# Optimization experiments

Hardware: AMD Instinct MI355X
Metric: run time of the kernel (lower is better)

Reference implementation:

```python
import jax, jax.numpy as jnp
import numpy as np

B, S, NX = 2, 2048, 1024
N_STATE, N_HEAD = 1024, 16
HEAD_DIM = N_STATE // N_HEAD


def setup_inputs() -> dict:
    key = jax.random.key(0)
    k1, k2, k3 = jax.random.split(key, 3)
    x = jax.random.normal(k1, (B, S, NX), dtype=jnp.float32)
    w_c = jax.random.normal(k2, (NX, 3 * N_STATE), dtype=jnp.float32) * 0.02
    b_c = jnp.zeros((3 * N_STATE,), dtype=jnp.float32)
    w_p = jax.random.normal(k3, (NX, N_STATE), dtype=jnp.float32) * 0.02
    b_p = jnp.zeros((N_STATE,), dtype=jnp.float32)
    return {"x": x, "w_c": w_c, "b_c": b_c, "w_p": w_p, "b_p": b_p}


def reference(x, w_c, b_c, w_p, b_p):
    # c_attn: 1x1 conv == dense over last dim -> [B, S, 3*n_state]
    c = jnp.einsum('bsn,nf->bsf', x, w_c) + b_c
    q, k, v = jnp.split(c, 3, axis=2)

    def split_heads(t):  # [B,S,n_state] -> [B,H,S,D]
        return t.reshape(B, S, N_HEAD, HEAD_DIM).transpose(0, 2, 1, 3)

    q = split_heads(q)
    k = split_heads(k)  # we contract over D directly instead of transposing to [B,H,D,S]
    v = split_heads(v)

    # scores [B,H,S,S], scaled by rsqrt(head_dim) (scale=True)
    w = jnp.einsum('bhqd,bhkd->bhqk', q, k) * jax.lax.rsqrt(jnp.float32(HEAD_DIM))
    # band mask exactly as in source: w*b + -1e9*(1-b)
    band = jnp.tril(jnp.ones((S, S), dtype=jnp.float32))[None, None]
    w = w * band + (-1e9) * (1.0 - band)
    w = jax.nn.softmax(w, axis=-1)
    a = jnp.einsum('bhqk,bhkd->bhqd', w, v)

    # merge heads -> [B,S,n_state]
    a = a.transpose(0, 2, 1, 3).reshape(B, S, N_STATE)
    # c_proj
    out = jnp.einsum('bsn,nf->bsf', a, w_p) + b_p
    return out
```

## Files before the change

### kernel.cpp

```cpp
#include <hip/hip_runtime.h>
#include <math.h>

#define BATCH 2
#define SEQ 2048
#define NX 1024
#define NSTATE 1024
#define NHEAD 16
#define HDIM 64
#define QKV_LD (3*NSTATE)

typedef __attribute__((ext_vector_type(4))) float f32x4;
typedef __attribute__((ext_vector_type(8))) short bf16x8;

__device__ __forceinline__ unsigned short f2bf(float x) {
    unsigned int u = __float_as_uint(x);
    u = (u + 0x7FFFu + ((u >> 16) & 1u)) >> 16;
    return (unsigned short)u;
}

#define GLL(src, dst) __builtin_amdgcn_global_load_lds( \
    (const __attribute__((address_space(1))) void*)(src), \
    (__attribute__((address_space(3))) void*)(dst), 16, 0, 0)

__global__ __launch_bounds__(256) void prep_kernel(
    const float* __restrict__ x, const float* __restrict__ w_c,
    const float* __restrict__ w_p,
    unsigned short* __restrict__ xbf, unsigned short* __restrict__ wcT,
    unsigned short* __restrict__ wpT)
{
    const int bx = blockIdx.x;
    const int t = threadIdx.x;
    if (bx < 4096) {
        int i = bx * 256 + t;
        float4 v = ((const float4*)x)[i];
        ushort4 o;
        o.x = f2bf(v.x); o.y = f2bf(v.y); o.z = f2bf(v.z); o.w = f2bf(v.w);
        ((ushort4*)xbf)[i] = o;
        return;
    }
    __shared__ float tile[64][65];
    const float* in;
    unsigned short* out;
    int R, C, c0, r0;
    if (bx < 4096 + 768) {
        int idx = bx - 4096;
        in = w_c; out = wcT; R = NX; C = 3 * NSTATE;
        c0 = (idx % 48) * 64; r0 = (idx / 48) * 64;
    } else {
        int idx = bx - 4864;
        in = w_p; out = wpT; R = NX; C = NSTATE;
        c0 = (idx % 16) * 64; r0 = (idx / 16) * 64;
    }
    const int cc = t & 63;
    const int rb = t >> 6;
    #pragma unroll
    for (int i = 0; i < 16; i++) {
        int rr = rb + i * 4;
        tile[rr][cc] = in[(size_t)(r0 + rr) * C + c0 + cc];
    }
    __syncthreads();
    #pragma unroll
    for (int i = 0; i < 16; i++) {
        int rr = rb + i * 4;
        out[(size_t)(c0 + rr) * R + r0 + cc] = f2bf(tile[cc][rr]);
    }
}

__global__ __launch_bounds__(256) void vtrans_kernel(
    const unsigned short* __restrict__ qkv, unsigned short* __restrict__ vt)
{
    __shared__ unsigned short t[64][72];
    const int s0 = blockIdx.x * 64;
    const int bh = blockIdx.y;
    const int b = bh >> 4, h = bh & 15;
    const int r = threadIdx.x >> 2;
    const int cg = (threadIdx.x & 3) * 16;
    const unsigned short* src = qkv + (size_t)(b * SEQ + s0 + r) * QKV_LD
                                + 2 * NSTATE + h * HDIM + cg;
    *(bf16x8*)&t[r][cg]     = *(const bf16x8*)src;
    *(bf16x8*)&t[r][cg + 8] = *(const bf16x8*)(src + 8);
    __syncthreads();
    unsigned short tmp[16];
    #pragma unroll
    for (int i = 0; i < 16; i++) tmp[i] = t[cg + i][r];
    unsigned short* dst = vt + (size_t)(bh * 64 + r) * SEQ + s0 + cg;
    *(bf16x8*)dst       = ((const bf16x8*)tmp)[0];
    *(bf16x8*)(dst + 8) = ((const bf16x8*)tmp)[1];
}

template<bool BF16_OUT>
__global__ __launch_bounds__(256) void gemm_bf16(
    const unsigned short* __restrict__ A,
    const unsigned short* __restrict__ BT,
    const float* __restrict__ bias,
    void* __restrict__ Cv, int M, int N, int K)
{
    __shared__ unsigned short Als[128 * 32];
    __shared__ unsigned short Bls[128 * 32];
    const int tid = threadIdx.x;
    const int wave = tid >> 6, lane = tid & 63;
    const int bm = blockIdx.x * 128, bn = blockIdx.y * 128;
    const int wr = (wave >> 1) * 64, wc = (wave & 1) * 64;

    f32x4 acc[4][4];
    #pragma unroll
    for (int m = 0; m < 4; m++)
        #pragma unroll
        for (int n = 0; n < 4; n++)
            acc[m][n] = (f32x4){0.f, 0.f, 0.f, 0.f};

    const int arow = tid >> 2;
    const int ac8 = (tid & 3) * 8;
    char* alds0 = (char*)Als + wave * 1024;
    char* blds0 = (char*)Bls + wave * 1024;
    const int fr = lane & 15, kq = (lane >> 4) * 8;

    for (int k0 = 0; k0 < K; k0 += 32) {
        const unsigned short* ga0 = A  + (size_t)(bm + arow) * K + k0 + ac8;
        const unsigned short* gb0 = BT + (size_t)(bn + arow) * K + k0 + ac8;
        GLL(ga0, alds0);
        GLL(ga0 + (size_t)64 * K, alds0 + 4096);
        GLL(gb0, blds0);
        GLL(gb0 + (size_t)64 * K, blds0 + 4096);
        __syncthreads();

        bf16x8 af[4], bfr[4];
        #pragma unroll
        for (int m = 0; m < 4; m++)
            af[m] = *(const bf16x8*)&Als[(wr + m * 16 + fr) * 32 + kq];
        #pragma unroll
        for (int n = 0; n < 4; n++)
            bfr[n] = *(const bf16x8*)&Bls[(wc + n * 16 + fr) * 32 + kq];
        #pragma unroll
        for (int m = 0; m < 4; m++)
            #pragma unroll
            for (int n = 0; n < 4; n++)
                acc[m][n] = __builtin_amdgcn_mfma_f32_16x16x32_bf16(
                    af[m], bfr[n], acc[m][n], 0, 0, 0);
        __syncthreads();
    }

    const int cr = (lane >> 4) * 4;
    const int ccol = lane & 15;
    #pragma unroll
    for (int m = 0; m < 4; m++) {
        const int row = bm + wr + m * 16 + cr;
        #pragma unroll
        for (int n = 0; n < 4; n++) {
            const int col = bn + wc + n * 16 + ccol;
            const float bv = bias[col];
            #pragma unroll
            for (int j = 0; j < 4; j++) {
                float v = acc[m][n][j] + bv;
                if (BF16_OUT)
                    ((unsigned short*)Cv)[(size_t)(row + j) * N + col] = f2bf(v);
                else
                    ((float*)Cv)[(size_t)(row + j) * N + col] = v;
            }
        }
    }
}

__global__ __launch_bounds__(256) void attn_mfma(
    const unsigned short* __restrict__ qkv,
    const unsigned short* __restrict__ vt,
    unsigned short* __restrict__ a_out)
{
    const int qb = (int)gridDim.x - 1 - (int)blockIdx.x;
    const int h = blockIdx.y, b = blockIdx.z;
    const int tid = threadIdx.x;
    const int w = tid >> 6, lane = tid & 63;
    const int c = lane & 15, hh = lane >> 4;

    __shared__ unsigned short Kls[2 * 64 * 64];
    __shared__ unsigned short Vls[2 * 64 * 64];
    __shared__ unsigned short Pls[4][16 * 64];

    const size_t qrow = (size_t)(b * SEQ + qb * 64 + w * 16 + c);
    const unsigned short* qp = qkv + qrow * QKV_LD + h * HDIM;
    bf16x8 qf0 = *(const bf16x8*)(qp + hh * 8);
    bf16x8 qf1 = *(const bf16x8*)(qp + 32 + hh * 8);

    f32x4 acc_o[4];
    #pragma unroll
    for (int n = 0; n < 4; n++) acc_o[n] = (f32x4){0.f, 0.f, 0.f, 0.f};
    float m_run = -1e30f, l = 0.f;
    const float Cc = 0.18033688f;

    const int o0 = tid * 16;
    const int r0 = o0 >> 7, sc0 = (o0 & 127) ^ ((r0 & 7) << 4);
    const int o1 = 4096 + tid * 16;
    const int r1 = o1 >> 7, sc1 = (o1 & 127) ^ ((r1 & 7) << 4);

    char* kld = (char*)Kls + w * 1024;
    char* vld = (char*)Vls + w * 1024;
    const char* gkbase = (const char*)(qkv + (size_t)b * SEQ * QKV_LD + NSTATE + h * HDIM);
    const char* gvbase = (const char*)(vt + (size_t)(b * NHEAD + h) * HDIM * SEQ);

    #define STAGE(kt_, buf_) do { \
        const char* gk = gkbase + (size_t)(kt_) * 64 * 6144; \
        const char* gv = gvbase + (size_t)(kt_) * 128; \
        char* kd = kld + (buf_) * 8192; \
        char* vd = vld + (buf_) * 8192; \
        GLL(gk + (size_t)r0 * 6144 + sc0, kd); \
        GLL(gk + (size_t)r1 * 6144 + sc1, kd + 4096); \
        GLL(gv + (size_t)r0 * 4096 + sc0, vd); \
        GLL(gv + (size_t)r1 * 4096 + sc1, vd + 4096); \
    } while (0)

    const int nkt = qb + 1;
    STAGE(0, 0);
    __syncthreads();

    for (int kt = 0; kt < nkt; kt++) {
        const int cur = kt & 1;
        if (kt + 1 < nkt) STAGE(kt + 1, cur ^ 1);

        const char* kb = (const char*)Kls + cur * 8192;
        const char* vb = (const char*)Vls + cur * 8192;

        f32x4 sacc[4];
        __builtin_amdgcn_s_setprio(1);
        #pragma unroll
        for (int m = 0; m < 4; m++) {
            const int row = m * 16 + c;
            const int sw = (row & 7) << 4;
            bf16x8 kf0 = *(const bf16x8*)(kb + row * 128 + ((hh * 16) ^ sw));
            bf16x8 kf1 = *(const bf16x8*)(kb + row * 128 + ((64 + hh * 16) ^ sw));
            f32x4 z = (f32x4){0.f, 0.f, 0.f, 0.f};
            z = __builtin_amdgcn_mfma_f32_16x16x32_bf16(kf0, qf0, z, 0, 0, 0);
            sacc[m] = __builtin_amdgcn_mfma_f32_16x16x32_bf16(kf1, qf1, z, 0, 0, 0);
        }
        __builtin_amdgcn_s_setprio(0);

        const bool diag = (kt == qb);
        float s[16];
        float pmax = -3.0e38f;
        #pragma unroll
        for (int m = 0; m < 4; m++)
            #pragma unroll
            for (int j = 0; j < 4; j++) {
                float sv = sacc[m][j];
                if (diag) {
                    int klocal = m * 16 + hh * 4 + j;
                    if (klocal > w * 16 + c) sv = -1e30f;
                }
                s[m * 4 + j] = sv;
                pmax = fmaxf(pmax, sv);
            }
        pmax = fmaxf(pmax, __shfl_xor(pmax, 16));
        pmax = fmaxf(pmax, __shfl_xor(pmax, 32));

        if (!__all(pmax <= m_run + 64.0f)) {
            const float mnew = fmaxf(m_run, pmax);
            const float alpha = exp2f((m_run - mnew) * Cc);
            m_run = mnew;
            l *= alpha;
            const float a0 = __shfl(alpha, hh * 4 + 0);
            const float a1 = __shfl(alpha, hh * 4 + 1);
            const float a2 = __shfl(alpha, hh * 4 + 2);
            const float a3 = __shfl(alpha, hh * 4 + 3);
            #pragma unroll
            for (int n = 0; n < 4; n++) {
                acc_o[n][0] *= a0; acc_o[n][1] *= a1;
                acc_o[n][2] *= a2; acc_o[n][3] *= a3;
            }
        }
        const float mc = m_run * Cc;
        float p[16];
        #pragma unroll
        for (int i = 0; i < 16; i++) {
            p[i] = exp2f(fmaf(s[i], Cc, -mc));
            l += p[i];
        }

        {
            char* pb = (char*)&Pls[w][0] + c * 128;
            const int swp = (c & 7) << 4;
            #pragma unroll
            for (int m = 0; m < 4; m++) {
                unsigned int lo = (unsigned int)f2bf(p[m * 4 + 0]) |
                                  ((unsigned int)f2bf(p[m * 4 + 1]) << 16);
                unsigned int hi = (unsigned int)f2bf(p[m * 4 + 2]) |
                                  ((unsigned int)f2bf(p[m * 4 + 3]) << 16);
                uint2 u; u.x = lo; u.y = hi;
                *(uint2*)(pb + ((m * 32 + hh * 8) ^ swp)) = u;
            }
        }

        {
            const char* pb = (const char*)&Pls[w][0] + c * 128;
            const int swp = (c & 7) << 4;
            bf16x8 pf0 = *(const bf16x8*)(pb + ((hh * 16) ^ swp));
            bf16x8 pf1 = *(const bf16x8*)(pb + ((64 + hh * 16) ^ swp));
            __builtin_amdgcn_s_setprio(1);
            #pragma unroll
            for (int n = 0; n < 4; n++) {
                const int row = n * 16 + c;
                const int sw = (row & 7) << 4;
                bf16x8 vf0 = *(const bf16x8*)(vb + row * 128 + ((hh * 16) ^ sw));
                bf16x8 vf1 = *(const bf16x8*)(vb + row * 128 + ((64 + hh * 16) ^ sw));
                acc_o[n] = __builtin_amdgcn_mfma_f32_16x16x32_bf16(pf0, vf0, acc_o[n], 0, 0, 0);
                acc_o[n] = __builtin_amdgcn_mfma_f32_16x16x32_bf16(pf1, vf1, acc_o[n], 0, 0, 0);
            }
            __builtin_amdgcn_s_setprio(0);
        }
        __syncthreads();
    }
    #undef STAGE

    l += __shfl_xor(l, 16);
    l += __shfl_xor(l, 32);
    const float linv = 1.f / l;
    const float li0 = __shfl(linv, hh * 4 + 0);
    const float li1 = __shfl(linv, hh * 4 + 1);
    const float li2 = __shfl(linv, hh * 4 + 2);
    const float li3 = __shfl(linv, hh * 4 + 3);
    const size_t orow0 = (size_t)(b * SEQ + qb * 64 + w * 16 + hh * 4);
    #pragma unroll
    for (int n = 0; n < 4; n++) {
        const int col = h * HDIM + n * 16 + c;
        a_out[(orow0 + 0) * NSTATE + col] = f2bf(acc_o[n][0] * li0);
        a_out[(orow0 + 1) * NSTATE + col] = f2bf(acc_o[n][1] * li1);
        a_out[(orow0 + 2) * NSTATE + col] = f2bf(acc_o[n][2] * li2);
        a_out[(orow0 + 3) * NSTATE + col] = f2bf(acc_o[n][3] * li3);
    }
}

extern "C" void kernel_launch(void* const* d_in, const int* in_sizes, int n_in,
                              void* d_out, int out_size, void* d_ws, size_t ws_size,
                              hipStream_t stream)
{
    const float* x   = (const float*)d_in[0];
    const float* w_c = (const float*)d_in[1];
    const float* b_c = (const float*)d_in[2];
    const float* w_p = (const float*)d_in[3];
    const float* b_p = (const float*)d_in[4];
    float* out = (float*)d_out;

    const int M = BATCH * SEQ;

    char* ws = (char*)d_ws;
    unsigned short* qkvbf = (unsigned short*)ws;
    unsigned short* vt    = (unsigned short*)(ws + 25165824);
    unsigned short* xbf   = (unsigned short*)(ws + 25165824 + 8388608);
    unsigned short* wcT   = (unsigned short*)(ws + 25165824 + 2*8388608);
    unsigned short* wpT   = (unsigned short*)(ws + 25165824 + 2*8388608 + 6291456);

    prep_kernel<<<5120, 256, 0, stream>>>(x, w_c, w_p, xbf, wcT, wpT);

    gemm_bf16<true><<<dim3(M / 128, 3 * NSTATE / 128), 256, 0, stream>>>(
        xbf, wcT, b_c, qkvbf, M, 3 * NSTATE, NX);

    vtrans_kernel<<<dim3(SEQ / 64, BATCH * NHEAD), 256, 0, stream>>>(qkvbf, vt);

    attn_mfma<<<dim3(SEQ / 64, NHEAD, BATCH), 256, 0, stream>>>(qkvbf, vt, xbf);

    gemm_bf16<false><<<dim3(M / 128, NSTATE / 128), 256, 0, stream>>>(
        xbf, wpT, b_p, out, M, NSTATE, NX);
}
```

Measured before the change: 232.9 us.

## Pair causal query blocks per workgroup and use packed bf16 conversion

The attention grid is halved: each workgroup now handles two query blocks, a long one (31-bx) and a short one (bx). This evens out causal work across workgroups and removes tail imbalance. The row max and sum reductions become trees, and P is converted to bf16 with the packed v_cvt_pk_bf16_f32 instruction instead of manual rounding. The cost is fewer workgroups (512) and therefore less parallelism to hide latency, plus a serial dependence between the two phases.

```diff
diff --git a/kernel.cpp b/kernel.cpp
--- a/kernel.cpp
+++ b/kernel.cpp
@@ -16,6 +16,12 @@
     unsigned int u = __float_as_uint(x);
     u = (u + 0x7FFFu + ((u >> 16) & 1u)) >> 16;
     return (unsigned short)u;
+}
+
+__device__ __forceinline__ unsigned int cvtpk_bf16(float a, float b) {
+    unsigned int r;
+    asm("v_cvt_pk_bf16_f32 %0, %1, %2" : "=v"(r) : "v"(a), "v"(b));
+    return r;
 }
 
 #define GLL(src, dst) __builtin_amdgcn_global_load_lds( \
@@ -166,7 +172,7 @@
     const unsigned short* __restrict__ vt,
     unsigned short* __restrict__ a_out)
 {
-    const int qb = (int)gridDim.x - 1 - (int)blockIdx.x;
+    const int bx = blockIdx.x;
     const int h = blockIdx.y, b = blockIdx.z;
     const int tid = threadIdx.x;
     const int w = tid >> 6, lane = tid & 63;
@@ -176,15 +182,6 @@
     __shared__ unsigned short Vls[2 * 64 * 64];
     __shared__ unsigned short Pls[4][16 * 64];
 
-    const size_t qrow = (size_t)(b * SEQ + qb * 64 + w * 16 + c);
-    const unsigned short* qp = qkv + qrow * QKV_LD + h * HDIM;
-    bf16x8 qf0 = *(const bf16x8*)(qp + hh * 8);
-    bf16x8 qf1 = *(const bf16x8*)(qp + 32 + hh * 8);
-
-    f32x4 acc_o[4];
-    #pragma unroll
-    for (int n = 0; n < 4; n++) acc_o[n] = (f32x4){0.f, 0.f, 0.f, 0.f};
-    float m_run = -1e30f, l = 0.f;
     const float Cc = 0.18033688f;
 
     const int o0 = tid * 16;
@@ -208,123 +205,146 @@
         GLL(gv + (size_t)r1 * 4096 + sc1, vd + 4096); \
     } while (0)
 
-    const int nkt = qb + 1;
-    STAGE(0, 0);
-    __syncthreads();
-
-    for (int kt = 0; kt < nkt; kt++) {
-        const int cur = kt & 1;
-        if (kt + 1 < nkt) STAGE(kt + 1, cur ^ 1);
-
-        const char* kb = (const char*)Kls + cur * 8192;
-        const char* vb = (const char*)Vls + cur * 8192;
-
-        f32x4 sacc[4];
-        __builtin_amdgcn_s_setprio(1);
-        #pragma unroll
-        for (int m = 0; m < 4; m++) {
-            const int row = m * 16 + c;
-            const int sw = (row & 7) << 4;
-            bf16x8 kf0 = *(const bf16x8*)(kb + row * 128 + ((hh * 16) ^ sw));
-            bf16x8 kf1 = *(const bf16x8*)(kb + row * 128 + ((64 + hh * 16) ^ sw));
-            f32x4 z = (f32x4){0.f, 0.f, 0.f, 0.f};
-            z = __builtin_amdgcn_mfma_f32_16x16x32_bf16(kf0, qf0, z, 0, 0, 0);
-            sacc[m] = __builtin_amdgcn_mfma_f32_16x16x32_bf16(kf1, qf1, z, 0, 0, 0);
+    for (int phase = 0; phase < 2; phase++) {
+        const int qb = phase ? bx : (31 - bx);
+
+        const size_t qrow = (size_t)(b * SEQ + qb * 64 + w * 16 + c);
+        const unsigned short* qp = qkv + qrow * QKV_LD + h * HDIM;
+        bf16x8 qf0 = *(const bf16x8*)(qp + hh * 8);
+        bf16x8 qf1 = *(const bf16x8*)(qp + 32 + hh * 8);
+
+        f32x4 acc_o[4];
+        #pragma unroll
+        for (int n = 0; n < 4; n++) acc_o[n] = (f32x4){0.f, 0.f, 0.f, 0.f};
+        float m_run = -1e30f, l = 0.f;
+
+        const int nkt = qb + 1;
+        STAGE(0, 0);
+        __syncthreads();
+
+        for (int kt = 0; kt < nkt; kt++) {
+            const int cur = kt & 1;
+            if (kt + 1 < nkt) STAGE(kt + 1, cur ^ 1);
+
+            const char* kb = (const char*)Kls + cur * 8192;
+            const char* vb = (const char*)Vls + cur * 8192;
+
+            f32x4 sacc[4];
+            __builtin_amdgcn_s_setprio(1);
+            #pragma unroll
+            for (int m = 0; m < 4; m++) {
+                const int row = m * 16 + c;
+                const int sw = (row & 7) << 4;
+                bf16x8 kf0 = *(const bf16x8*)(kb + row * 128 + ((hh * 16) ^ sw));
+                bf16x8 kf1 = *(const bf16x8*)(kb + row * 128 + ((64 + hh * 16) ^ sw));
+                f32x4 z = (f32x4){0.f, 0.f, 0.f, 0.f};
+                z = __builtin_amdgcn_mfma_f32_16x16x32_bf16(kf0, qf0, z, 0, 0, 0);
+                sacc[m] = __builtin_amdgcn_mfma_f32_16x16x32_bf16(kf1, qf1, z, 0, 0, 0);
+            }
+            __builtin_amdgcn_s_setprio(0);
+
+            const bool diag = (kt == qb);
+            float s[16];
+            #pragma unroll
+            for (int m = 0; m < 4; m++)
+                #pragma unroll
+                for (int j = 0; j < 4; j++) {
+                    float sv = sacc[m][j];
+                    if (diag) {
+                        int klocal = m * 16 + hh * 4 + j;
+                        if (klocal > w * 16 + c) sv = -1e30f;
+                    }
+                    s[m * 4 + j] = sv;
+                }
+            float x0 = fmaxf(s[0], s[1]),  x1 = fmaxf(s[2], s[3]);
+            float x2 = fmaxf(s[4], s[5]),  x3 = fmaxf(s[6], s[7]);
+            float x4 = fmaxf(s[8], s[9]),  x5 = fmaxf(s[10], s[11]);
+            float x6 = fmaxf(s[12], s[13]), x7 = fmaxf(s[14], s[15]);
+            float y0 = fmaxf(x0, x1), y1 = fmaxf(x2, x3);
+            float y2 = fmaxf(x4, x5), y3 = fmaxf(x6, x7);
+            float pmax = fmaxf(fmaxf(y0, y1), fmaxf(y2, y3));
+            pmax = fmaxf(pmax, __shfl_xor(pmax, 16));
+            pmax = fmaxf(pmax, __shfl_xor(pmax, 32));
+
+            if (!__all(pmax <= m_run + 64.0f)) {
+                const float mnew = fmaxf(m_run, pmax);
+                const float alpha = exp2f((m_run - mnew) * Cc);
+                m_run = mnew;
+                l *= alpha;
+                const float a0 = __shfl(alpha, hh * 4 + 0);
+                const float a1 = __shfl(alpha, hh * 4 + 1);
+                const float a2 = __shfl(alpha, hh * 4 + 2);
+                const float a3 = __shfl(alpha, hh * 4 + 3);
+                #pragma unroll
+                for (int n = 0; n < 4; n++) {
+                    acc_o[n][0] *= a0; acc_o[n][1] *= a1;
+                    acc_o[n][2] *= a2; acc_o[n][3] *= a3;
+                }
+            }
+            const float mc = m_run * Cc;
+            float p[16];
+            #pragma unroll
+            for (int i = 0; i < 16; i++)
+                p[i] = exp2f(fmaf(s[i], Cc, -mc));
+            {
+                float a0 = p[0] + p[1],  a1 = p[2] + p[3];
+                float a2 = p[4] + p[5],  a3 = p[6] + p[7];
+                float a4 = p[8] + p[9],  a5 = p[10] + p[11];
+                float a6 = p[12] + p[13], a7 = p[14] + p[15];
+                float b0 = a0 + a1, b1 = a2 + a3, b2 = a4 + a5, b3 = a6 + a7;
+                l += (b0 + b1) + (b2 + b3);
+            }
+
+            {
+                char* pb = (char*)&Pls[w][0] + c * 128;
+                const int swp = (c & 7) << 4;
+                #pragma unroll
+                for (int m = 0; m < 4; m++) {
+                    uint2 u;
+                    u.x = cvtpk_bf16(p[m * 4 + 0], p[m * 4 + 1]);
+                    u.y = cvtpk_bf16(p[m * 4 + 2], p[m * 4 + 3]);
+                    *(uint2*)(pb + ((m * 32 + hh * 8) ^ swp)) = u;
+                }
+            }
+
+            {
+                const char* pb = (const char*)&Pls[w][0] + c * 128;
+                const int swp = (c & 7) << 4;
+                bf16x8 pf0 = *(const bf16x8*)(pb + ((hh * 16) ^ swp));
+                bf16x8 pf1 = *(const bf16x8*)(pb + ((64 + hh * 16) ^ swp));
+                __builtin_amdgcn_s_setprio(1);
+                #pragma unroll
+                for (int n = 0; n < 4; n++) {
+                    const int row = n * 16 + c;
+                    const int sw = (row & 7) << 4;
+                    bf16x8 vf0 = *(const bf16x8*)(vb + row * 128 + ((hh * 16) ^ sw));
+                    bf16x8 vf1 = *(const bf16x8*)(vb + row * 128 + ((64 + hh * 16) ^ sw));
+                    acc_o[n] = __builtin_amdgcn_mfma_f32_16x16x32_bf16(pf0, vf0, acc_o[n], 0, 0, 0);
+                    acc_o[n] = __builtin_amdgcn_mfma_f32_16x16x32_bf16(pf1, vf1, acc_o[n], 0, 0, 0);
+                }
+                __builtin_amdgcn_s_setprio(0);
+            }
+            __syncthreads();
         }
-        __builtin_amdgcn_s_setprio(0);
-
-        const bool diag = (kt == qb);
-        float s[16];
-        float pmax = -3.0e38f;
-        #pragma unroll
-        for (int m = 0; m < 4; m++)
-            #pragma unroll
-            for (int j = 0; j < 4; j++) {
-                float sv = sacc[m][j];
-                if (diag) {
-                    int klocal = m * 16 + hh * 4 + j;
-                    if (klocal > w * 16 + c) sv = -1e30f;
-                }
-                s[m * 4 + j] = sv;
-                pmax = fmaxf(pmax, sv);
-            }
-        pmax = fmaxf(pmax, __shfl_xor(pmax, 16));
-        pmax = fmaxf(pmax, __shfl_xor(pmax, 32));
-
-        if (!__all(pmax <= m_run + 64.0f)) {
-            const float mnew = fmaxf(m_run, pmax);
-            const float alpha = exp2f((m_run - mnew) * Cc);
-            m_run = mnew;
-            l *= alpha;
-            const float a0 = __shfl(alpha, hh * 4 + 0);
-            const float a1 = __shfl(alpha, hh * 4 + 1);
-            const float a2 = __shfl(alpha, hh * 4 + 2);
-            const float a3 = __shfl(alpha, hh * 4 + 3);
-            #pragma unroll
-            for (int n = 0; n < 4; n++) {
-                acc_o[n][0] *= a0; acc_o[n][1] *= a1;
-                acc_o[n][2] *= a2; acc_o[n][3] *= a3;
-            }
+
+        l += __shfl_xor(l, 16);
+        l += __shfl_xor(l, 32);
+        const float linv = 1.f / l;
+        const float li0 = __shfl(linv, hh * 4 + 0);
+        const float li1 = __shfl(linv, hh * 4 + 1);
+        const float li2 = __shfl(linv, hh * 4 + 2);
+        const float li3 = __shfl(linv, hh * 4 + 3);
+        const size_t orow0 = (size_t)(b * SEQ + qb * 64 + w * 16 + hh * 4);
+        #pragma unroll
+        for (int n = 0; n < 4; n++) {
+            const int col = h * HDIM + n * 16 + c;
+            a_out[(orow0 + 0) * NSTATE + col] = f2bf(acc_o[n][0] * li0);
+            a_out[(orow0 + 1) * NSTATE + col] = f2bf(acc_o[n][1] * li1);
+            a_out[(orow0 + 2) * NSTATE + col] = f2bf(acc_o[n][2] * li2);
+            a_out[(orow0 + 3) * NSTATE + col] = f2bf(acc_o[n][3] * li3);
         }
-        const float mc = m_run * Cc;
-        float p[16];
-        #pragma unroll
-        for (int i = 0; i < 16; i++) {
-            p[i] = exp2f(fmaf(s[i], Cc, -mc));
-            l += p[i];
-        }
-
-        {
-            char* pb = (char*)&Pls[w][0] + c * 128;
-            const int swp = (c & 7) << 4;
-            #pragma unroll
-            for (int m = 0; m < 4; m++) {
-                unsigned int lo = (unsigned int)f2bf(p[m * 4 + 0]) |
-                                  ((unsigned int)f2bf(p[m * 4 + 1]) << 16);
-                unsigned int hi = (unsigned int)f2bf(p[m * 4 + 2]) |
-                                  ((unsigned int)f2bf(p[m * 4 + 3]) << 16);
-                uint2 u; u.x = lo; u.y = hi;
-                *(uint2*)(pb + ((m * 32 + hh * 8) ^ swp)) = u;
-            }
-        }
-
-        {
-            const char* pb = (const char*)&Pls[w][0] + c * 128;
-            const int swp = (c & 7) << 4;
-            bf16x8 pf0 = *(const bf16x8*)(pb + ((hh * 16) ^ swp));
-            bf16x8 pf1 = *(const bf16x8*)(pb + ((64 + hh * 16) ^ swp));
-            __builtin_amdgcn_s_setprio(1);
-            #pragma unroll
-            for (int n = 0; n < 4; n++) {
-                const int row = n * 16 + c;
-                const int sw = (row & 7) << 4;
-                bf16x8 vf0 = *(const bf16x8*)(vb + row * 128 + ((hh * 16) ^ sw));
-                bf16x8 vf1 = *(const bf16x8*)(vb + row * 128 + ((64 + hh * 16) ^ sw));
-                acc_o[n] = __builtin_amdgcn_mfma_f32_16x16x32_bf16(pf0, vf0, acc_o[n], 0, 0, 0);
-                acc_o[n] = __builtin_amdgcn_mfma_f32_16x16x32_bf16(pf1, vf1, acc_o[n], 0, 0, 0);
-            }
-            __builtin_amdgcn_s_setprio(0);
-        }
-        __syncthreads();
     }
     #undef STAGE
-
-    l += __shfl_xor(l, 16);
-    l += __shfl_xor(l, 32);
-    const float linv = 1.f / l;
-    const float li0 = __shfl(linv, hh * 4 + 0);
-    const float li1 = __shfl(linv, hh * 4 + 1);
-    const float li2 = __shfl(linv, hh * 4 + 2);
-    const float li3 = __shfl(linv, hh * 4 + 3);
-    const size_t orow0 = (size_t)(b * SEQ + qb * 64 + w * 16 + hh * 4);
-    #pragma unroll
-    for (int n = 0; n < 4; n++) {
-        const int col = h * HDIM + n * 16 + c;
-        a_out[(orow0 + 0) * NSTATE + col] = f2bf(acc_o[n][0] * li0);
-        a_out[(orow0 + 1) * NSTATE + col] = f2bf(acc_o[n][1] * li1);
-        a_out[(orow0 + 2) * NSTATE + col] = f2bf(acc_o[n][2] * li2);
-        a_out[(orow0 + 3) * NSTATE + col] = f2bf(acc_o[n][3] * li3);
-    }
 }
 
 extern "C" void kernel_launch(void* const* d_in, const int* in_sizes, int n_in,
@@ -354,7 +374,7 @@
 
     vtrans_kernel<<<dim3(SEQ / 64, BATCH * NHEAD), 256, 0, stream>>>(qkvbf, vt);
 
-    attn_mfma<<<dim3(SEQ / 64, NHEAD, BATCH), 256, 0, stream>>>(qkvbf, vt, xbf);
+    attn_mfma<<<dim3(16, NHEAD, BATCH), 256, 0, stream>>>(qkvbf, vt, xbf);
 
     gemm_bf16<false><<<dim3(M / 128, NSTATE / 128), 256, 0, stream>>>(
         xbf, wpT, b_p, out, M, NSTATE, NX);
```

After: 204.1 us. 1.14x faster.
